# Kernel optimization log

Measured on AMD Instinct MI355X. Metric: run time of the kernel, lower is better.

Reference implementation:

```python
import jax, jax.numpy as jnp
import numpy as np

N_GAUSS = 2048
HEIGHT = 192
WIDTH = 192
ALPHA_MAX = 0.999
ALPHA_MIN = 1.0 / 255.0


def setup_inputs() -> dict:
    key = jax.random.key(0)
    k1, k2, k3, k4, k5, k6 = jax.random.split(key, 6)
    # 2D means in pixel coords
    means2d = jax.random.uniform(k1, (N_GAUSS, 2)) * jnp.array([WIDTH, HEIGHT], jnp.float32)
    depths = jax.random.uniform(k2, (N_GAUSS,)) * 10.0 + 0.1
    # build positive-definite 2x2 pixel-space covariances -> conics (inverse cov)
    scales = jax.random.uniform(k3, (N_GAUSS, 2)) * 6.0 + 1.0  # std 1..7 px
    theta = jax.random.uniform(k4, (N_GAUSS,)) * (2.0 * np.pi)
    c, s = jnp.cos(theta), jnp.sin(theta)
    s0, s1 = scales[:, 0] ** 2, scales[:, 1] ** 2
    cxx = c * c * s0 + s * s * s1
    cyy = s * s * s0 + c * c * s1
    cxy = c * s * (s0 - s1)
    det = cxx * cyy - cxy * cxy
    conics = jnp.stack([cyy / det, -cxy / det, cxx / det], axis=-1)  # [a,b,c]
    colors = jax.random.uniform(k5, (N_GAUSS, 3))
    opacities = jax.random.uniform(k6, (N_GAUSS,)) * 0.9 + 0.05
    background = jnp.zeros((3,), jnp.float32)
    return {"means2d": means2d, "conics": conics, "colors": colors,
            "opacities": opacities, "depths": depths, "background": background}


def reference(means2d, conics, colors, opacities, depths, background):
    # depth sort (front to back), as gsplat's tile sort does globally per image
    order = jnp.argsort(depths)
    means2d = means2d[order]
    conics = conics[order]
    colors = colors[order]
    opacities = opacities[order]

    # pixel centers, flattened to P = H*W
    ys, xs = jnp.meshgrid(jnp.arange(HEIGHT, dtype=jnp.float32) + 0.5,
                          jnp.arange(WIDTH, dtype=jnp.float32) + 0.5,
                          indexing="ij")
    px = xs.reshape(-1)  # [P]
    py = ys.reshape(-1)

    dx = px[None, :] - means2d[:, 0:1]  # [N, P]
    dy = py[None, :] - means2d[:, 1:2]
    a, b, cc = conics[:, 0:1], conics[:, 1:2], conics[:, 2:3]
    # gsplat 2DGS fallback: sigma = 0.5*(A dx^2 + C dy^2) + B dx dy
    sigma = 0.5 * (a * dx * dx + cc * dy * dy) + b * dx * dy
    alpha = jnp.minimum(ALPHA_MAX, opacities[:, None] * jnp.exp(-sigma))
    alpha = jnp.where((sigma > 0.0) & (alpha >= ALPHA_MIN), alpha, 0.0)

    one_minus = 1.0 - alpha
    trans = jnp.cumprod(one_minus, axis=0)  # inclusive
    # exclusive transmittance before each gaussian
    T = jnp.concatenate([jnp.ones((1, alpha.shape[1]), alpha.dtype), trans[:-1]], axis=0)
    w = T * alpha  # [N, P] compositing weights
    rgb = jnp.einsum("np,nc->cp", w, colors)  # [3, P]
    T_final = trans[-1]  # [P]
    img = rgb + background[:, None] * T_final[None, :]
    return img.reshape(3, HEIGHT, WIDTH)
```

## Files before the change

### kernel.cpp

```cpp
#include <hip/hip_runtime.h>
#include <hip/hip_bf16.h>

#define NG 2048
#define IMW 192
#define IMH 192
#define CHUNK 256
#define KPT (NG / 512)

__device__ __forceinline__ float bf2f(unsigned short u) {
    union { unsigned int i; float f; } v;
    v.i = ((unsigned int)u) << 16;
    return v.f;
}

__device__ __forceinline__ unsigned short f2bf(float f) {
    union { float f; unsigned int i; } v;
    v.f = f;
    unsigned int x = v.i;
    unsigned int r = (x + 0x7fffu + ((x >> 16) & 1u)) >> 16;
    return (unsigned short)r;
}

__device__ __forceinline__ bool probe_is_f32_wave(const unsigned short* dus, int lane) {
    float v = bf2f(dus[lane & 63]);
    bool bad = !(v >= 0.05f && v <= 16.0f);
    return __ballot(bad) != 0ull;
}

__global__ __launch_bounds__(512) void fused_render_kernel(
    const void* __restrict__ means2d_,
    const void* __restrict__ conics_,
    const void* __restrict__ colors_,
    const void* __restrict__ opac_,
    const void* __restrict__ depths_,
    const void* __restrict__ background_,
    void* __restrict__ out_)
{
    __shared__ unsigned long long s_keys[NG];
    __shared__ float4 s_pay[(CHUNK + 1) * 3];
    __shared__ float4 s_comb[8][64];
    __shared__ float4 s_run[64];
    __shared__ unsigned int s_cnt;
    __shared__ int s_stop;

    const int t    = threadIdx.x;
    const int lane = t & 63;
    const int wave = t >> 6;
    const unsigned short* dus = (const unsigned short*)depths_;
    const bool is_f32 = probe_is_f32_wave(dus, lane);

    const int bx = blockIdx.x % 24;
    const int by = blockIdx.x / 24;
    const float cx = (float)(bx * 8) + 4.0f;
    const float cy = (float)(by * 8) + 4.0f;
    const int x = bx * 8 + (lane & 7);
    const int y = by * 8 + (lane >> 3);
    const float px = (float)x + 0.5f;
    const float py = (float)y + 0.5f;

    if (t == 0) { s_cnt = 0u; s_stop = 0; }
    if (t < 64) s_run[t] = make_float4(0.f, 0.f, 0.f, 1.f);
    __syncthreads();

#pragma unroll
    for (int k = 0; k < KPT; ++k) {
        const int g = t + k * 512;
        float mx, my, ca, cb, cc, op;
        unsigned int dbits;
        if (is_f32) {
            const float2* mf2 = (const float2*)means2d_;
            const float* cf = (const float*)conics_;
            const float* of = (const float*)opac_;
            const unsigned int* du = (const unsigned int*)depths_;
            const float2 mxy = mf2[g];
            mx = mxy.x; my = mxy.y;
            ca = cf[3 * g]; cb = cf[3 * g + 1]; cc = cf[3 * g + 2];
            op = of[g];
            dbits = du[g];
        } else {
            const unsigned int* mu2 = (const unsigned int*)means2d_;
            const unsigned short* cu = (const unsigned short*)conics_;
            const unsigned short* ou = (const unsigned short*)opac_;
            const unsigned int mxy = mu2[g];
            mx = bf2f((unsigned short)(mxy & 0xffffu));
            my = bf2f((unsigned short)(mxy >> 16));
            ca = bf2f(cu[3 * g]); cb = bf2f(cu[3 * g + 1]); cc = bf2f(cu[3 * g + 2]);
            op = bf2f(ou[g]);
            dbits = ((unsigned int)dus[g]) << 16;
        }

        const float det = ca * cc - cb * cb;
        const float tau = __logf(255.0f * op);
        bool hit;
        if (det > 1e-12f && tau > 0.0f) {
            const float s = 2.0f * tau / det;
            const float rx = __fsqrt_rn(fmaxf(s * cc, 0.0f)) + 3.55f;
            const float ry = __fsqrt_rn(fmaxf(s * ca, 0.0f)) + 3.55f;
            hit = (__builtin_fabsf(mx - cx) <= rx) && (__builtin_fabsf(my - cy) <= ry);
        } else if (tau <= 0.0f) {
            hit = false;
        } else {
            hit = true;
        }
        const unsigned long long bal = __ballot(hit);
        if (hit) {
            const unsigned int prefix =
                (unsigned int)__popcll(bal & ((1ull << lane) - 1ull));
            unsigned int base = 0u;
            if (prefix == 0u)
                base = atomicAdd(&s_cnt, (unsigned int)__popcll(bal));
            base = (unsigned int)__shfl((int)base, (int)__builtin_ctzll(bal));
            s_keys[base + prefix] =
                (((unsigned long long)dbits) << 32) | (unsigned long long)g;
        }
    }
    __syncthreads();
    const int n = (int)s_cnt;

    unsigned long long mykey[KPT];
    int myrank[KPT];
#pragma unroll
    for (int j = 0; j < KPT; ++j) {
        const int i = t + j * 512;
        mykey[j] = (i < n) ? s_keys[i] : ~0ull;
        myrank[j] = 0;
    }
    if (t < n) {
        int k = 0;
        for (; k + 8 <= n; k += 8) {
            const unsigned long long k0 = s_keys[k + 0];
            const unsigned long long k1 = s_keys[k + 1];
            const unsigned long long k2 = s_keys[k + 2];
            const unsigned long long k3 = s_keys[k + 3];
            const unsigned long long k4 = s_keys[k + 4];
            const unsigned long long k5 = s_keys[k + 5];
            const unsigned long long k6 = s_keys[k + 6];
            const unsigned long long k7 = s_keys[k + 7];
#pragma unroll
            for (int j = 0; j < KPT; ++j) {
                const unsigned long long mk = mykey[j];
                int r = myrank[j];
                r += (k0 < mk) ? 1 : 0;
                r += (k1 < mk) ? 1 : 0;
                r += (k2 < mk) ? 1 : 0;
                r += (k3 < mk) ? 1 : 0;
                r += (k4 < mk) ? 1 : 0;
                r += (k5 < mk) ? 1 : 0;
                r += (k6 < mk) ? 1 : 0;
                r += (k7 < mk) ? 1 : 0;
                myrank[j] = r;
            }
        }
        for (; k < n; ++k) {
            const unsigned long long kk = s_keys[k];
#pragma unroll
            for (int j = 0; j < KPT; ++j)
                myrank[j] += (kk < mykey[j]) ? 1 : 0;
        }
    }
    __syncthreads();
#pragma unroll
    for (int j = 0; j < KPT; ++j)
        if (t + j * 512 < n) s_keys[myrank[j]] = mykey[j];
    __syncthreads();

    const float L2E = 1.44269504088896f;
    for (int cb0 = 0; cb0 < n; cb0 += CHUNK) {
        const int m = min(CHUNK, n - cb0);

        if (t < m) {
            const int g = (int)(s_keys[cb0 + t] & 0xffffffffull);
            float mx, my, ca, cb, cc, op, r0, g0, b0;
            if (is_f32) {
                const float2* mf2 = (const float2*)means2d_;
                const float* cf = (const float*)conics_;
                const float* lf = (const float*)colors_;
                const float* of = (const float*)opac_;
                const float2 mxy = mf2[g];
                mx = mxy.x; my = mxy.y;
                ca = cf[3 * g]; cb = cf[3 * g + 1]; cc = cf[3 * g + 2];
                r0 = lf[3 * g]; g0 = lf[3 * g + 1]; b0 = lf[3 * g + 2];
                op = of[g];
            } else {
                const unsigned int* mu2 = (const unsigned int*)means2d_;
                const unsigned short* cu = (const unsigned short*)conics_;
                const unsigned short* lu = (const unsigned short*)colors_;
                const unsigned short* ou = (const unsigned short*)opac_;
                const unsigned int mxy = mu2[g];
                mx = bf2f((unsigned short)(mxy & 0xffffu));
                my = bf2f((unsigned short)(mxy >> 16));
                ca = bf2f(cu[3 * g]); cb = bf2f(cu[3 * g + 1]); cc = bf2f(cu[3 * g + 2]);
                r0 = bf2f(lu[3 * g]); g0 = bf2f(lu[3 * g + 1]); b0 = bf2f(lu[3 * g + 2]);
                op = bf2f(ou[g]);
            }
            s_pay[t * 3 + 0] = make_float4(mx, my, 0.f, 0.f);
            s_pay[t * 3 + 1] = make_float4(0.5f * ca * L2E, cb * L2E, 0.5f * cc * L2E, __log2f(op));
            s_pay[t * 3 + 2] = make_float4(r0, g0, b0, 0.f);
        }
        __syncthreads();

        const int sl = (m + 7) >> 3;
        const int lo = wave * sl;
        const int hi = min(lo + sl, m);
        float T = 1.0f, ar = 0.f, ag = 0.f, ab = 0.f;
        if (lo < hi) {
            float4 h0 = s_pay[lo * 3 + 0];
            float4 h1 = s_pay[lo * 3 + 1];
            float4 h2 = s_pay[lo * 3 + 2];
            for (int k = lo; k < hi; ++k) {
                const float4 n0 = s_pay[(k + 1) * 3 + 0];
                const float4 n1 = s_pay[(k + 1) * 3 + 1];
                const float4 n2 = s_pay[(k + 1) * 3 + 2];
                const float dx = px - h0.x;
                const float dy = py - h0.y;
                const float sp = fmaf(h1.x * dx, dx, fmaf(h1.z * dy, dy, h1.y * dx * dy));
                const float e = h1.w - sp;
                const float alpha = __builtin_amdgcn_exp2f(e);
                const bool ok = (sp > 0.0f) && (e >= -7.9943534f);
                const float w = ok ? T * alpha : 0.0f;
                ar = fmaf(w, h2.x, ar);
                ag = fmaf(w, h2.y, ag);
                ab = fmaf(w, h2.z, ab);
                T -= w;
                h0 = n0; h1 = n1; h2 = n2;
            }
        }
        s_comb[wave][lane] = make_float4(ar, ag, ab, T);
        __syncthreads();

        if (t < 64) {
            float4 R = s_run[t];
#pragma unroll
            for (int w = 0; w < 8; ++w) {
                const float4 c = s_comb[w][t];
                R.x = fmaf(R.w, c.x, R.x);
                R.y = fmaf(R.w, c.y, R.y);
                R.z = fmaf(R.w, c.z, R.z);
                R.w *= c.w;
            }
            s_run[t] = R;
            if (__ballot(R.w > 1e-3f) == 0ull && t == 0) s_stop = 1;
        }
        __syncthreads();
        if (s_stop) break;
    }

    if (t < 64) {
        const float4 R = s_run[t];
        const int pix = y * IMW + x;
        if (is_f32) {
            const float* bg = (const float*)background_;
            float* out = (float*)out_;
            out[0 * IMH * IMW + pix] = fmaf(bg[0], R.w, R.x);
            out[1 * IMH * IMW + pix] = fmaf(bg[1], R.w, R.y);
            out[2 * IMH * IMW + pix] = fmaf(bg[2], R.w, R.z);
        } else {
            const unsigned short* bg = (const unsigned short*)background_;
            unsigned short* out = (unsigned short*)out_;
            out[0 * IMH * IMW + pix] = f2bf(fmaf(bf2f(bg[0]), R.w, R.x));
            out[1 * IMH * IMW + pix] = f2bf(fmaf(bf2f(bg[1]), R.w, R.y));
            out[2 * IMH * IMW + pix] = f2bf(fmaf(bf2f(bg[2]), R.w, R.z));
        }
    }
}

extern "C" void kernel_launch(void* const* d_in, const int* in_sizes, int n_in,
                              void* d_out, int out_size, void* d_ws, size_t ws_size,
                              hipStream_t stream)
{
    fused_render_kernel<<<576, 512, 0, stream>>>(
        d_in[0], d_in[1], d_in[2], d_in[3], d_in[4], d_in[5], d_out);
}
```

Baseline: 71.93 us.

## Add fast path for small per-tile lists: stage payload at cull, split composite across waves

```diff
diff --git a/kernel.cpp b/kernel.cpp
--- a/kernel.cpp
+++ b/kernel.cpp
@@ -36,7 +36,8 @@
     const void* __restrict__ background_,
     void* __restrict__ out_)
 {
-    __shared__ unsigned long long s_keys[NG];
+    __shared__ __align__(16) unsigned long long s_keys[NG];
+    __shared__ float4 s_payU[CHUNK * 3];
     __shared__ float4 s_pay[(CHUNK + 1) * 3];
     __shared__ float4 s_comb[8][64];
     __shared__ float4 s_run[64];
@@ -57,6 +58,8 @@
     const int y = by * 8 + (lane >> 3);
     const float px = (float)x + 0.5f;
     const float py = (float)y + 0.5f;
+
+    const float L2E = 1.44269504088896f;
 
     if (t == 0) { s_cnt = 0u; s_stop = 0; }
     if (t < 64) s_run[t] = make_float4(0.f, 0.f, 0.f, 1.f);
@@ -110,12 +113,27 @@
             if (prefix == 0u)
                 base = atomicAdd(&s_cnt, (unsigned int)__popcll(bal));
             base = (unsigned int)__shfl((int)base, (int)__builtin_ctzll(bal));
-            s_keys[base + prefix] =
+            const unsigned int slot = base + prefix;
+            s_keys[slot] =
                 (((unsigned long long)dbits) << 32) | (unsigned long long)g;
+            if (slot < CHUNK) {
+                float r0, g0, b0;
+                if (is_f32) {
+                    const float* lf = (const float*)colors_;
+                    r0 = lf[3 * g]; g0 = lf[3 * g + 1]; b0 = lf[3 * g + 2];
+                } else {
+                    const unsigned short* lu = (const unsigned short*)colors_;
+                    r0 = bf2f(lu[3 * g]); g0 = bf2f(lu[3 * g + 1]); b0 = bf2f(lu[3 * g + 2]);
+                }
+                s_payU[slot * 3 + 0] = make_float4(mx, my, 0.f, 0.f);
+                s_payU[slot * 3 + 1] = make_float4(0.5f * ca * L2E, cb * L2E, 0.5f * cc * L2E, __log2f(op));
+                s_payU[slot * 3 + 2] = make_float4(r0, g0, b0, 0.f);
+            }
         }
     }
     __syncthreads();
     const int n = (int)s_cnt;
+    const bool fast = (n <= CHUNK);
 
     unsigned long long mykey[KPT];
     int myrank[KPT];
@@ -126,28 +144,25 @@
         myrank[j] = 0;
     }
     if (t < n) {
+        const ulonglong2* kp = (const ulonglong2*)s_keys;
         int k = 0;
         for (; k + 8 <= n; k += 8) {
-            const unsigned long long k0 = s_keys[k + 0];
-            const unsigned long long k1 = s_keys[k + 1];
-            const unsigned long long k2 = s_keys[k + 2];
-            const unsigned long long k3 = s_keys[k + 3];
-            const unsigned long long k4 = s_keys[k + 4];
-            const unsigned long long k5 = s_keys[k + 5];
-            const unsigned long long k6 = s_keys[k + 6];
-            const unsigned long long k7 = s_keys[k + 7];
+            const ulonglong2 p0 = kp[(k >> 1) + 0];
+            const ulonglong2 p1 = kp[(k >> 1) + 1];
+            const ulonglong2 p2 = kp[(k >> 1) + 2];
+            const ulonglong2 p3 = kp[(k >> 1) + 3];
 #pragma unroll
             for (int j = 0; j < KPT; ++j) {
                 const unsigned long long mk = mykey[j];
                 int r = myrank[j];
-                r += (k0 < mk) ? 1 : 0;
-                r += (k1 < mk) ? 1 : 0;
-                r += (k2 < mk) ? 1 : 0;
-                r += (k3 < mk) ? 1 : 0;
-                r += (k4 < mk) ? 1 : 0;
-                r += (k5 < mk) ? 1 : 0;
-                r += (k6 < mk) ? 1 : 0;
-                r += (k7 < mk) ? 1 : 0;
+                r += (p0.x < mk) ? 1 : 0;
+                r += (p0.y < mk) ? 1 : 0;
+                r += (p1.x < mk) ? 1 : 0;
+                r += (p1.y < mk) ? 1 : 0;
+                r += (p2.x < mk) ? 1 : 0;
+                r += (p2.y < mk) ? 1 : 0;
+                r += (p3.x < mk) ? 1 : 0;
+                r += (p3.y < mk) ? 1 : 0;
                 myrank[j] = r;
             }
         }
@@ -159,12 +174,82 @@
         }
     }
     __syncthreads();
+
+    if (fast) {
+#pragma unroll
+        for (int j = 0; j < KPT; ++j) {
+            const int i = t + j * 512;
+            if (i < n) {
+                const int r = myrank[j];
+                s_pay[r * 3 + 0] = s_payU[i * 3 + 0];
+                s_pay[r * 3 + 1] = s_payU[i * 3 + 1];
+                s_pay[r * 3 + 2] = s_payU[i * 3 + 2];
+            }
+        }
+        __syncthreads();
+
+        const int sl = (n + 7) >> 3;
+        const int lo = wave * sl;
+        const int hi = min(lo + sl, n);
+        float T = 1.0f, ar = 0.f, ag = 0.f, ab = 0.f;
+        if (lo < hi) {
+            float4 h0 = s_pay[lo * 3 + 0];
+            float4 h1 = s_pay[lo * 3 + 1];
+            float4 h2 = s_pay[lo * 3 + 2];
+            for (int k = lo; k < hi; ++k) {
+                const float4 n0 = s_pay[(k + 1) * 3 + 0];
+                const float4 n1 = s_pay[(k + 1) * 3 + 1];
+                const float4 n2 = s_pay[(k + 1) * 3 + 2];
+                const float dx = px - h0.x;
+                const float dy = py - h0.y;
+                const float sp = fmaf(h1.x * dx, dx, fmaf(h1.z * dy, dy, h1.y * dx * dy));
+                const float e = h1.w - sp;
+                const float alpha = __builtin_amdgcn_exp2f(e);
+                const bool ok = (sp > 0.0f) && (e >= -7.9943534f);
+                const float w = ok ? T * alpha : 0.0f;
+                ar = fmaf(w, h2.x, ar);
+                ag = fmaf(w, h2.y, ag);
+                ab = fmaf(w, h2.z, ab);
+                T -= w;
+                h0 = n0; h1 = n1; h2 = n2;
+            }
+        }
+        s_comb[wave][lane] = make_float4(ar, ag, ab, T);
+        __syncthreads();
+
+        if (t < 64) {
+            float4 R = make_float4(0.f, 0.f, 0.f, 1.f);
+#pragma unroll
+            for (int w = 0; w < 8; ++w) {
+                const float4 c = s_comb[w][t];
+                R.x = fmaf(R.w, c.x, R.x);
+                R.y = fmaf(R.w, c.y, R.y);
+                R.z = fmaf(R.w, c.z, R.z);
+                R.w *= c.w;
+            }
+            const int pix = y * IMW + x;
+            if (is_f32) {
+                const float* bg = (const float*)background_;
+                float* out = (float*)out_;
+                out[0 * IMH * IMW + pix] = fmaf(bg[0], R.w, R.x);
+                out[1 * IMH * IMW + pix] = fmaf(bg[1], R.w, R.y);
+                out[2 * IMH * IMW + pix] = fmaf(bg[2], R.w, R.z);
+            } else {
+                const unsigned short* bg = (const unsigned short*)background_;
+                unsigned short* out = (unsigned short*)out_;
+                out[0 * IMH * IMW + pix] = f2bf(fmaf(bf2f(bg[0]), R.w, R.x));
+                out[1 * IMH * IMW + pix] = f2bf(fmaf(bf2f(bg[1]), R.w, R.y));
+                out[2 * IMH * IMW + pix] = f2bf(fmaf(bf2f(bg[2]), R.w, R.z));
+            }
+        }
+        return;
+    }
+
 #pragma unroll
     for (int j = 0; j < KPT; ++j)
         if (t + j * 512 < n) s_keys[myrank[j]] = mykey[j];
     __syncthreads();
 
-    const float L2E = 1.44269504088896f;
     for (int cb0 = 0; cb0 < n; cb0 += CHUNK) {
         const int m = min(CHUNK, n - cb0);
 
```

Measured after the change: 72.37 us. Within noise of the previous version (+0.6%).
